# Kernel tuning notes

Hardware: AMD Instinct MI355X
Metric: run time of the kernel (lower is better)

Reference implementation:

```python
import jax, jax.numpy as jnp
import numpy as np

N_HEADS, N_LEVELS, N_POINTS = 8, 4, 4
SPATIAL_SHAPES = np.array([[100, 100], [50, 50], [25, 25], [13, 13]], dtype=np.int32)


def setup_inputs() -> dict:
    key = jax.random.key(0)
    ks = jax.random.split(key, 6)
    N, Lq, C = 8, 4096, 256
    L_total = int(SPATIAL_SHAPES.prod(1).sum())  # 13294
    HLP = N_HEADS * N_LEVELS * N_POINTS  # 128
    return {
        "query": jax.random.normal(ks[0], (Lq, N, C), jnp.float32),
        "reference_points": jax.random.uniform(ks[1], (N, Lq, N_LEVELS, 2), jnp.float32),
        "feature_maps": jax.random.normal(ks[2], (L_total, N, C), jnp.float32),
        "spatial_shapes": SPATIAL_SHAPES,  # static numpy: drives reshapes
        "W_off": jax.random.normal(ks[3], (C, HLP * 2), jnp.float32) * 0.02,
        "b_off": jnp.zeros((HLP * 2,), jnp.float32),
        "W_attn": jax.random.normal(ks[4], (C, HLP), jnp.float32) * 0.02,
        "b_attn": jnp.zeros((HLP,), jnp.float32),
        "W_out": jax.random.normal(ks[5], (C, C), jnp.float32) / np.sqrt(C).astype(np.float32),
        "b_out": jnp.zeros((C,), jnp.float32),
    }


def bilinear_sample(img, gx, gy):
    """F.grid_sample(mode='bilinear', padding_mode='zeros', align_corners=False).
    img: (B, C, H, W); gx, gy: (B, P) normalized coords in [-1, 1]. -> (B, C, P)"""
    B, C, H, W = img.shape
    x = ((gx + 1.0) * W - 1.0) * 0.5
    y = ((gy + 1.0) * H - 1.0) * 0.5
    x0f = jnp.floor(x)
    y0f = jnp.floor(y)
    wx = x - x0f
    wy = y - y0f
    x0 = x0f.astype(jnp.int32)
    y0 = y0f.astype(jnp.int32)
    img_flat = img.reshape(B, C, H * W)

    def gather(ix, iy):
        valid = (ix >= 0) & (ix < W) & (iy >= 0) & (iy < H)
        idx = jnp.clip(iy, 0, H - 1) * W + jnp.clip(ix, 0, W - 1)  # (B, P)
        v = jax.vmap(lambda f, i: f[:, i])(img_flat, idx)  # (B, C, P)
        return v * valid[:, None, :].astype(img.dtype)

    v00 = gather(x0, y0)
    v01 = gather(x0 + 1, y0)
    v10 = gather(x0, y0 + 1)
    v11 = gather(x0 + 1, y0 + 1)
    w00 = ((1 - wx) * (1 - wy))[:, None, :]
    w01 = (wx * (1 - wy))[:, None, :]
    w10 = ((1 - wx) * wy)[:, None, :]
    w11 = (wx * wy)[:, None, :]
    return v00 * w00 + v01 * w01 + v10 * w10 + v11 * w11


def deform_attn(query, reference_points, feature_maps, spatial_shapes,
                W_off, b_off, W_attn, b_attn, W_out, b_out):
    Lq, N, C = query.shape
    H_, L_, P_ = N_HEADS, N_LEVELS, N_POINTS
    dh = C // H_
    q = jnp.transpose(query, (1, 0, 2))  # (N, Lq, C)
    off = (q @ W_off + b_off).reshape(N, Lq, H_, L_, P_, 2)
    attn = jax.nn.softmax((q @ W_attn + b_attn).reshape(N, Lq, H_, L_ * P_), axis=-1)
    attn = attn.reshape(N, Lq, H_, L_, P_)
    ss = np.asarray(spatial_shapes)  # (L, 2) as (H, W), static
    ss_flip = jnp.asarray(ss[:, ::-1].astype(np.float32))  # (L, 2) as (W, H)
    # sampling locations in [0,1], then to [-1,1] grid coords
    loc = reference_points[:, :, None, :, None, :] + off / ss_flip[None, None, None, :, None, :]
    grid = 2.0 * loc - 1.0  # (N, Lq, H, L, P, 2)
    starts = np.concatenate([[0], np.cumsum(ss.prod(1))[:-1]])
    sampled = []
    for lid in range(L_):
        Hl, Wl = int(ss[lid, 0]), int(ss[lid, 1])
        s = int(starts[lid])
        fm = feature_maps[s:s + Hl * Wl]  # (Hl*Wl, N, C)
        img = jnp.transpose(fm, (1, 2, 0)).reshape(N * H_, dh, Hl, Wl)
        g = jnp.transpose(grid[:, :, :, lid], (0, 2, 1, 3, 4)).reshape(N * H_, Lq * P_, 2)
        v = bilinear_sample(img, g[..., 0], g[..., 1])  # (N*H, dh, Lq*P)
        v = v.reshape(N, H_, dh, Lq, P_)
        sampled.append(jnp.transpose(v, (0, 3, 1, 2, 4)))  # (N, Lq, H, dh, P)
    sv = jnp.stack(sampled, axis=4)  # (N, Lq, H, dh, L, P)
    out = (attn[:, :, :, None, :, :] * sv).sum(axis=(-1, -2)).reshape(N, Lq, C)
    out = out @ W_out + b_out
    return jnp.transpose(out, (1, 0, 2))  # (Lq, N, C)


def reference(query, reference_points, feature_maps, spatial_shapes,
              W_off, b_off, W_attn, b_attn, W_out, b_out):
    return deform_attn(query, reference_points, feature_maps, spatial_shapes,
                       W_off, b_off, W_attn, b_attn, W_out, b_out)
```

## Files before the change

### kernel.cpp

```cpp
#include <hip/hip_runtime.h>

typedef unsigned short u16;
typedef __attribute__((ext_vector_type(8))) __bf16 bf16x8;
typedef __attribute__((ext_vector_type(4))) float f32x4;
typedef __attribute__((ext_vector_type(4))) int   i32x4;

#define NLQ 32768
#define WPN (384*256)
#define WON (256*256)
#define FM4 6806528

static __device__ __forceinline__ u16 f2bf(float f) {
    unsigned u = __float_as_uint(f);
    return (u16)((u + 0x7fffu + ((u >> 16) & 1u)) >> 16);
}

__global__ __launch_bounds__(256) void prep_kernel(
    const float4* __restrict__ fm, ushort4* __restrict__ fmb,
    const float* __restrict__ W_off, const float* __restrict__ W_attn,
    const float* __restrict__ W_out,
    u16* __restrict__ wtp, u16* __restrict__ wto)
{
    const int b = blockIdx.x, t = threadIdx.x;
    if (b < 6647) {
        const int base = b * 1024 + t;
        float4 v[4];
#pragma unroll
        for (int j = 0; j < 4; ++j) v[j] = fm[base + j * 256];
#pragma unroll
        for (int j = 0; j < 4; ++j) {
            ushort4 r;
            r.x = f2bf(v[j].x); r.y = f2bf(v[j].y);
            r.z = f2bf(v[j].z); r.w = f2bf(v[j].w);
            fmb[base + j * 256] = r;
        }
    } else {
        const int wi = (b - 6647) * 256 + t;
        if (wi < WPN) {
            int j = wi >> 8, k = wi & 255;
            float v = (j < 256) ? W_off[k * 256 + j] : W_attn[k * 128 + (j - 256)];
            wtp[wi] = f2bf(v);
        } else {
            int wi2 = wi - WPN;
            int j = wi2 >> 8, k = wi2 & 255;
            wto[wi2] = f2bf(W_out[k * 256 + j]);
        }
    }
}

__global__ __launch_bounds__(256) void proj_gemm(
    const float* __restrict__ query, const u16* __restrict__ Bt,
    const float* __restrict__ b_off, const float* __restrict__ b_attn,
    float* __restrict__ C)
{
    const int t = threadIdx.x;
    const int wid = t >> 6, lane = t & 63;
    const int lr = lane & 15, lk = lane >> 4;
    const int mrow = blockIdx.x * 128 + (wid >> 1) * 64;
    const int ncol = blockIdx.y * 128 + (wid & 1) * 64;
    const int kO = lk * 8;

    const float* qrow[4];
#pragma unroll
    for (int mi = 0; mi < 4; ++mi) {
        int gq = mrow + mi * 16 + lr;
        qrow[mi] = query + (size_t)((gq & 4095) * 8 + (gq >> 12)) * 256;
    }

    f32x4 acc[4][4] = {};
#pragma unroll
    for (int kk = 0; kk < 8; ++kk) {
        bf16x8 a[4], b[4];
#pragma unroll
        for (int mi = 0; mi < 4; ++mi) {
            f32x4 lo = *(const f32x4*)(qrow[mi] + kk * 32 + kO);
            f32x4 hi = *(const f32x4*)(qrow[mi] + kk * 32 + kO + 4);
#pragma unroll
            for (int j = 0; j < 4; ++j) {
                a[mi][j]     = (__bf16)lo[j];
                a[mi][4 + j] = (__bf16)hi[j];
            }
        }
#pragma unroll
        for (int ni = 0; ni < 4; ++ni)
            b[ni] = *(const bf16x8*)(Bt + (size_t)(ncol + ni * 16 + lr) * 256 + kk * 32 + kO);
#pragma unroll
        for (int mi = 0; mi < 4; ++mi)
#pragma unroll
            for (int ni = 0; ni < 4; ++ni)
                acc[mi][ni] = __builtin_amdgcn_mfma_f32_16x16x32_bf16(a[mi], b[ni], acc[mi][ni], 0, 0, 0);
    }

#pragma unroll
    for (int ni = 0; ni < 4; ++ni) {
        int gcol = ncol + ni * 16 + lr;
        float bias = (gcol < 256) ? b_off[gcol] : b_attn[gcol - 256];
#pragma unroll
        for (int mi = 0; mi < 4; ++mi) {
            f32x4 v = acc[mi][ni];
#pragma unroll
            for (int r = 0; r < 4; ++r)
                C[(size_t)(mrow + mi * 16 + lk * 4 + r) * 384 + gcol] = v[r] + bias;
        }
    }
}

__global__ __launch_bounds__(256) void sample_kernel(
    const u16* __restrict__ fmb,
    const float* __restrict__ proj,
    const float* __restrict__ refp,
    u16* __restrict__ mid)
{
    __shared__ i32x4 loff[256];
    __shared__ f32x4 lwv[256];
    const int t = threadIdx.x;
    const int ql = t >> 7, pt = t & 127;
    const int gq = blockIdx.x * 2 + ql;
    const int n = gq >> 12;

    {
        const int lp = pt & 15, l = lp >> 2;
        float lg = proj[(size_t)gq * 384 + 256 + pt];
        float m = lg;
#pragma unroll
        for (int msk = 1; msk < 16; msk <<= 1) m = fmaxf(m, __shfl_xor(m, msk));
        float e = __expf(lg - m);
        float s = e;
#pragma unroll
        for (int msk = 1; msk < 16; msk <<= 1) s += __shfl_xor(s, msk);
        float a = e / s;

        float ox = proj[(size_t)gq * 384 + 2 * pt];
        float oy = proj[(size_t)gq * 384 + 2 * pt + 1];
        int   Sl = (l == 0) ? 100 : (l == 1) ? 50 : (l == 2) ? 25 : 13;
        int   lb = (l == 0) ? 0 : (l == 1) ? 10000 : (l == 2) ? 12500 : 13125;
        float Sf = (float)Sl;
        float rx = refp[((size_t)gq * 4 + l) * 2 + 0];
        float ry = refp[((size_t)gq * 4 + l) * 2 + 1];
        float px = rx * Sf + ox - 0.5f;
        float py = ry * Sf + oy - 0.5f;
        float x0f = floorf(px), y0f = floorf(py);
        float wx = px - x0f, wy = py - y0f;
        int x0 = (int)x0f, y0 = (int)y0f;
        bool xv0 = (unsigned)x0 < (unsigned)Sl;
        bool xv1 = (unsigned)(x0 + 1) < (unsigned)Sl;
        bool yv0 = (unsigned)y0 < (unsigned)Sl;
        bool yv1 = (unsigned)(y0 + 1) < (unsigned)Sl;
        int x0c = min(max(x0, 0), Sl - 1), x1c = min(max(x0 + 1, 0), Sl - 1);
        int y0c = min(max(y0, 0), Sl - 1), y1c = min(max(y0 + 1, 0), Sl - 1);
        int r0 = (lb + y0c * Sl) << 12, r1 = (lb + y1c * Sl) << 12;
        i32x4 o; f32x4 w;
        o.x = r0 + (x0c << 12); o.y = r0 + (x1c << 12);
        o.z = r1 + (x0c << 12); o.w = r1 + (x1c << 12);
        w.x = (xv0 && yv0) ? a * (1.f - wx) * (1.f - wy) : 0.f;
        w.y = (xv1 && yv0) ? a * wx * (1.f - wy) : 0.f;
        w.z = (xv0 && yv1) ? a * (1.f - wx) * wy : 0.f;
        w.w = (xv1 && yv1) ? a * wx * wy : 0.f;
        loff[t] = o;
        lwv[t] = w;
    }
    __syncthreads();

    const int h = pt >> 4, ll = pt & 15, g = ll >> 3, cq = ll & 7;
    const uint boff = (uint)(n * 512 + h * 64 + cq * 8);
    const char* __restrict__ fb = (const char*)fmb;

    float acc0 = 0.f, acc1 = 0.f, acc2 = 0.f, acc3 = 0.f;
#pragma unroll
    for (int bi = 0; bi < 2; ++bi) {
        uint2 v[4][4];
        f32x4 w[4];
#pragma unroll
        for (int pi = 0; pi < 4; ++pi) {
            int idx = ql * 128 + h * 16 + g * 8 + bi * 4 + pi;
            i32x4 o = loff[idx];
            w[pi] = lwv[idx];
            v[pi][0] = *(const uint2*)(fb + (boff + (uint)o.x));
            v[pi][1] = *(const uint2*)(fb + (boff + (uint)o.y));
            v[pi][2] = *(const uint2*)(fb + (boff + (uint)o.z));
            v[pi][3] = *(const uint2*)(fb + (boff + (uint)o.w));
        }
#pragma unroll
        for (int pi = 0; pi < 4; ++pi) {
#pragma unroll
            for (int cn = 0; cn < 4; ++cn) {
                float wt = w[pi][cn];
                uint2 u = v[pi][cn];
                acc0 += wt * __uint_as_float(u.x << 16);
                acc1 += wt * __uint_as_float(u.x & 0xFFFF0000u);
                acc2 += wt * __uint_as_float(u.y << 16);
                acc3 += wt * __uint_as_float(u.y & 0xFFFF0000u);
            }
        }
    }
    acc0 += __shfl_xor(acc0, 8);  acc1 += __shfl_xor(acc1, 8);
    acc2 += __shfl_xor(acc2, 8);  acc3 += __shfl_xor(acc3, 8);

    if (ll < 8) {
        ushort4 r;
        r.x = f2bf(acc0); r.y = f2bf(acc1);
        r.z = f2bf(acc2); r.w = f2bf(acc3);
        ((ushort4*)mid)[(size_t)gq * 64 + h * 8 + cq] = r;
    }
}

__global__ __launch_bounds__(256) void out_gemm(
    const u16* __restrict__ A, const u16* __restrict__ Bt,
    const float* __restrict__ b_out,
    float* __restrict__ out)
{
    const int t = threadIdx.x;
    const int wid = t >> 6, lane = t & 63;
    const int lr = lane & 15, lk = lane >> 4;
    const int mrow = blockIdx.x * 128 + (wid >> 1) * 64;
    const int ncol = blockIdx.y * 128 + (wid & 1) * 64;
    const int kO = lk * 8;

    f32x4 acc[4][4] = {};
#pragma unroll
    for (int kk = 0; kk < 8; ++kk) {
        bf16x8 a[4], b[4];
#pragma unroll
        for (int mi = 0; mi < 4; ++mi)
            a[mi] = *(const bf16x8*)(A + (size_t)(mrow + mi * 16 + lr) * 256 + kk * 32 + kO);
#pragma unroll
        for (int ni = 0; ni < 4; ++ni)
            b[ni] = *(const bf16x8*)(Bt + (size_t)(ncol + ni * 16 + lr) * 256 + kk * 32 + kO);
#pragma unroll
        for (int mi = 0; mi < 4; ++mi)
#pragma unroll
            for (int ni = 0; ni < 4; ++ni)
                acc[mi][ni] = __builtin_amdgcn_mfma_f32_16x16x32_bf16(a[mi], b[ni], acc[mi][ni], 0, 0, 0);
    }

#pragma unroll
    for (int ni = 0; ni < 4; ++ni) {
        int gcol = ncol + ni * 16 + lr;
        float bias = b_out[gcol];
#pragma unroll
        for (int mi = 0; mi < 4; ++mi) {
            f32x4 v = acc[mi][ni];
#pragma unroll
            for (int r = 0; r < 4; ++r) {
                int grow = mrow + mi * 16 + lk * 4 + r;
                int nn = grow >> 12, lq = grow & 4095;
                out[(size_t)(lq * 8 + nn) * 256 + gcol] = v[r] + bias;
            }
        }
    }
}

extern "C" void kernel_launch(void* const* d_in, const int* in_sizes, int n_in,
                              void* d_out, int out_size, void* d_ws, size_t ws_size,
                              hipStream_t stream) {
    const float* query  = (const float*)d_in[0];
    const float* refp   = (const float*)d_in[1];
    const float* fm     = (const float*)d_in[2];
    const float* W_off  = (const float*)d_in[4];
    const float* b_off  = (const float*)d_in[5];
    const float* W_attn = (const float*)d_in[6];
    const float* b_attn = (const float*)d_in[7];
    const float* W_out  = (const float*)d_in[8];
    const float* b_out  = (const float*)d_in[9];
    float* out = (float*)d_out;

    float* ws_proj = (float*)d_ws;
    u16*   wtp     = (u16*)(ws_proj + (size_t)NLQ * 384);
    u16*   wto     = wtp + (size_t)WPN;
    u16*   mid     = wto + (size_t)WON;
    u16*   fmb     = mid + (size_t)NLQ * 256;

    prep_kernel<<<6647 + 640, 256, 0, stream>>>((const float4*)fm, (ushort4*)fmb,
                                                W_off, W_attn, W_out, wtp, wto);
    proj_gemm<<<dim3(256, 3), 256, 0, stream>>>(query, wtp, b_off, b_attn, ws_proj);
    sample_kernel<<<NLQ / 2, 256, 0, stream>>>(fmb, ws_proj, refp, mid);
    out_gemm<<<dim3(256, 2), 256, 0, stream>>>(mid, wto, b_out, out);
}
```

Baseline: 171.9 us.

## Fuse feature-map bf16 conversion into projection GEMM launch and widen sampling loads

```diff
diff --git a/kernel.cpp b/kernel.cpp
--- a/kernel.cpp
+++ b/kernel.cpp
@@ -8,56 +8,59 @@
 #define NLQ 32768
 #define WPN (384*256)
 #define WON (256*256)
-#define FM4 6806528
+#define FMU 3403264
 
 static __device__ __forceinline__ u16 f2bf(float f) {
     unsigned u = __float_as_uint(f);
     return (u16)((u + 0x7fffu + ((u >> 16) & 1u)) >> 16);
 }
-
-__global__ __launch_bounds__(256) void prep_kernel(
-    const float4* __restrict__ fm, ushort4* __restrict__ fmb,
+static __device__ __forceinline__ uint pk2(float lo, float hi) {
+    return (uint)f2bf(lo) | ((uint)f2bf(hi) << 16);
+}
+
+__global__ __launch_bounds__(256) void wconv_kernel(
     const float* __restrict__ W_off, const float* __restrict__ W_attn,
     const float* __restrict__ W_out,
     u16* __restrict__ wtp, u16* __restrict__ wto)
 {
-    const int b = blockIdx.x, t = threadIdx.x;
-    if (b < 6647) {
-        const int base = b * 1024 + t;
-        float4 v[4];
-#pragma unroll
-        for (int j = 0; j < 4; ++j) v[j] = fm[base + j * 256];
-#pragma unroll
-        for (int j = 0; j < 4; ++j) {
-            ushort4 r;
-            r.x = f2bf(v[j].x); r.y = f2bf(v[j].y);
-            r.z = f2bf(v[j].z); r.w = f2bf(v[j].w);
-            fmb[base + j * 256] = r;
-        }
+    const int wi = blockIdx.x * 256 + threadIdx.x;
+    if (wi < WPN) {
+        int j = wi >> 8, k = wi & 255;
+        float v = (j < 256) ? W_off[k * 256 + j] : W_attn[k * 128 + (j - 256)];
+        wtp[wi] = f2bf(v);
     } else {
-        const int wi = (b - 6647) * 256 + t;
-        if (wi < WPN) {
-            int j = wi >> 8, k = wi & 255;
-            float v = (j < 256) ? W_off[k * 256 + j] : W_attn[k * 128 + (j - 256)];
-            wtp[wi] = f2bf(v);
-        } else {
-            int wi2 = wi - WPN;
-            int j = wi2 >> 8, k = wi2 & 255;
-            wto[wi2] = f2bf(W_out[k * 256 + j]);
-        }
-    }
-}
-
-__global__ __launch_bounds__(256) void proj_gemm(
+        int wi2 = wi - WPN;
+        int j = wi2 >> 8, k = wi2 & 255;
+        wto[wi2] = f2bf(W_out[k * 256 + j]);
+    }
+}
+
+__global__ __launch_bounds__(256) void fused_kernel(
     const float* __restrict__ query, const u16* __restrict__ Bt,
     const float* __restrict__ b_off, const float* __restrict__ b_attn,
-    float* __restrict__ C)
-{
-    const int t = threadIdx.x;
+    float* __restrict__ C,
+    const float4* __restrict__ fm, uint4* __restrict__ fmb)
+{
+    const int bx = blockIdx.x, t = threadIdx.x;
+    if (bx >= 768) {
+        const int ub = (bx - 768) * 1024 + t;
+#pragma unroll
+        for (int j = 0; j < 4; ++j) {
+            int u = ub + j * 256;
+            if (u < FMU) {
+                float4 lo = fm[2 * u], hi = fm[2 * u + 1];
+                uint4 r;
+                r.x = pk2(lo.x, lo.y); r.y = pk2(lo.z, lo.w);
+                r.z = pk2(hi.x, hi.y); r.w = pk2(hi.z, hi.w);
+                fmb[u] = r;
+            }
+        }
+        return;
+    }
     const int wid = t >> 6, lane = t & 63;
     const int lr = lane & 15, lk = lane >> 4;
-    const int mrow = blockIdx.x * 128 + (wid >> 1) * 64;
-    const int ncol = blockIdx.y * 128 + (wid & 1) * 64;
+    const int mrow = (bx & 255) * 128 + (wid >> 1) * 64;
+    const int ncol = (bx >> 8) * 128 + (wid & 1) * 64;
     const int kO = lk * 8;
 
     const float* qrow[4];
@@ -161,46 +164,46 @@
     }
     __syncthreads();
 
-    const int h = pt >> 4, ll = pt & 15, g = ll >> 3, cq = ll & 7;
-    const uint boff = (uint)(n * 512 + h * 64 + cq * 8);
+    const int h = pt >> 4, ll = pt & 15, g2 = ll >> 2, cl = ll & 3;
+    const uint boff = (uint)(n * 512 + h * 64 + cl * 16);
     const char* __restrict__ fb = (const char*)fmb;
 
-    float acc0 = 0.f, acc1 = 0.f, acc2 = 0.f, acc3 = 0.f;
-#pragma unroll
-    for (int bi = 0; bi < 2; ++bi) {
-        uint2 v[4][4];
-        f32x4 w[4];
-#pragma unroll
-        for (int pi = 0; pi < 4; ++pi) {
-            int idx = ql * 128 + h * 16 + g * 8 + bi * 4 + pi;
-            i32x4 o = loff[idx];
-            w[pi] = lwv[idx];
-            v[pi][0] = *(const uint2*)(fb + (boff + (uint)o.x));
-            v[pi][1] = *(const uint2*)(fb + (boff + (uint)o.y));
-            v[pi][2] = *(const uint2*)(fb + (boff + (uint)o.z));
-            v[pi][3] = *(const uint2*)(fb + (boff + (uint)o.w));
-        }
-#pragma unroll
-        for (int pi = 0; pi < 4; ++pi) {
-#pragma unroll
-            for (int cn = 0; cn < 4; ++cn) {
-                float wt = w[pi][cn];
-                uint2 u = v[pi][cn];
-                acc0 += wt * __uint_as_float(u.x << 16);
-                acc1 += wt * __uint_as_float(u.x & 0xFFFF0000u);
-                acc2 += wt * __uint_as_float(u.y << 16);
-                acc3 += wt * __uint_as_float(u.y & 0xFFFF0000u);
-            }
-        }
-    }
-    acc0 += __shfl_xor(acc0, 8);  acc1 += __shfl_xor(acc1, 8);
-    acc2 += __shfl_xor(acc2, 8);  acc3 += __shfl_xor(acc3, 8);
-
-    if (ll < 8) {
-        ushort4 r;
-        r.x = f2bf(acc0); r.y = f2bf(acc1);
-        r.z = f2bf(acc2); r.w = f2bf(acc3);
-        ((ushort4*)mid)[(size_t)gq * 64 + h * 8 + cq] = r;
+    float a0 = 0.f, a1 = 0.f, a2 = 0.f, a3 = 0.f;
+    float a4 = 0.f, a5 = 0.f, a6 = 0.f, a7 = 0.f;
+#pragma unroll
+    for (int pi = 0; pi < 4; ++pi) {
+        int idx = ql * 128 + h * 16 + g2 * 4 + pi;
+        i32x4 o = loff[idx];
+        f32x4 w = lwv[idx];
+        uint4 v0 = *(const uint4*)(fb + (boff + (uint)o.x));
+        uint4 v1 = *(const uint4*)(fb + (boff + (uint)o.y));
+        uint4 v2 = *(const uint4*)(fb + (boff + (uint)o.z));
+        uint4 v3 = *(const uint4*)(fb + (boff + (uint)o.w));
+#define ACC8(u, wt)                                        \
+        a0 += wt * __uint_as_float(u.x << 16);             \
+        a1 += wt * __uint_as_float(u.x & 0xFFFF0000u);     \
+        a2 += wt * __uint_as_float(u.y << 16);             \
+        a3 += wt * __uint_as_float(u.y & 0xFFFF0000u);     \
+        a4 += wt * __uint_as_float(u.z << 16);             \
+        a5 += wt * __uint_as_float(u.z & 0xFFFF0000u);     \
+        a6 += wt * __uint_as_float(u.w << 16);             \
+        a7 += wt * __uint_as_float(u.w & 0xFFFF0000u);
+        ACC8(v0, w.x) ACC8(v1, w.y) ACC8(v2, w.z) ACC8(v3, w.w)
+#undef ACC8
+    }
+#pragma unroll
+    for (int msk = 4; msk <= 8; msk <<= 1) {
+        a0 += __shfl_xor(a0, msk); a1 += __shfl_xor(a1, msk);
+        a2 += __shfl_xor(a2, msk); a3 += __shfl_xor(a3, msk);
+        a4 += __shfl_xor(a4, msk); a5 += __shfl_xor(a5, msk);
+        a6 += __shfl_xor(a6, msk); a7 += __shfl_xor(a7, msk);
+    }
+
+    if (ll < 4) {
+        uint4 r;
+        r.x = pk2(a0, a1); r.y = pk2(a2, a3);
+        r.z = pk2(a4, a5); r.w = pk2(a6, a7);
+        ((uint4*)mid)[(size_t)gq * 32 + h * 4 + cl] = r;
     }
 }
 
@@ -270,9 +273,10 @@
     u16*   mid     = wto + (size_t)WON;
     u16*   fmb     = mid + (size_t)NLQ * 256;
 
-    prep_kernel<<<6647 + 640, 256, 0, stream>>>((const float4*)fm, (ushort4*)fmb,
-                                                W_off, W_attn, W_out, wtp, wto);
-    proj_gemm<<<dim3(256, 3), 256, 0, stream>>>(query, wtp, b_off, b_attn, ws_proj);
+    wconv_kernel<<<640, 256, 0, stream>>>(W_off, W_attn, W_out, wtp, wto);
+    fused_kernel<<<768 + 3324, 256, 0, stream>>>(query, wtp, b_off, b_attn,
+                                                 ws_proj, (const float4*)fm,
+                                                 (uint4*)fmb);
     sample_kernel<<<NLQ / 2, 256, 0, stream>>>(fmb, ws_proj, refp, mid);
     out_gemm<<<dim3(256, 2), 256, 0, stream>>>(mid, wto, b_out, out);
 }
```

After: 161.3 us. -6.1%, faster.
